# Optimization experiments

Hardware: AMD Instinct MI355X
Metric: run time of the kernel (lower is better)

## Reference

```python
import jax, jax.numpy as jnp
import numpy as np

N = 100000
E = 3200000
IN_C, HID, OUT_C = 256, 32, 16


def gcn_conv(x, W, b, src, dst, n):
    """PyG GCNConv: h = D^{-1/2}(A+I)D^{-1/2} (x W) + b, self-loops already in src/dst."""
    h = x @ W  # [N, out]
    deg = jax.ops.segment_sum(jnp.ones_like(dst, dtype=h.dtype), dst, num_segments=n)
    dinv = jax.lax.rsqrt(deg)  # deg >= 1 because of self-loops
    norm = dinv[src] * dinv[dst]  # [E_all]
    msg = h[src] * norm[:, None]  # gather + normalize
    return jax.ops.segment_sum(msg, dst, num_segments=n) + b


def setup_inputs() -> dict:
    key = jax.random.key(0)
    k1, k2, k3, k4 = jax.random.split(key, 4)
    x = jax.random.normal(k1, (N, IN_C), dtype=jnp.float32)
    edge_index = jax.random.randint(k2, (2, E), 0, N, dtype=jnp.int64)
    # Glorot-ish init for weights, zero bias (as in PyG defaults)
    W1 = jax.random.normal(k3, (IN_C, HID), dtype=jnp.float32) / np.sqrt(IN_C)
    b1 = jnp.zeros((HID,), dtype=jnp.float32)
    W2 = jax.random.normal(k4, (HID, OUT_C), dtype=jnp.float32) / np.sqrt(HID)
    b2 = jnp.zeros((OUT_C,), dtype=jnp.float32)
    return {"x": x, "edge_index": edge_index, "W1": W1, "b1": b1, "W2": W2, "b2": b2}


def reference(x, edge_index, W1, b1, W2, b2):
    n = x.shape[0]
    loops = jnp.arange(n, dtype=edge_index.dtype)
    src = jnp.concatenate([edge_index[0], loops])  # add self-loops
    dst = jnp.concatenate([edge_index[1], loops])
    h = jax.nn.relu(gcn_conv(x, W1, b1, src, dst, n))
    return gcn_conv(h, W2, b2, src, dst, n)
```

## Files before the change

### kernel.cpp

```cpp
#include <hip/hip_runtime.h>

#define IN_C 256
#define HIDC 32
#define OUTC 16
#define NPB  256
#define MAXBKT 800
#define CAP  16384
#define EPB  12288
#define EPT  12

typedef __attribute__((ext_vector_type(8))) short short8;
typedef __attribute__((ext_vector_type(4))) float f32x4;
union S8U4 { short8 s; unsigned u[4]; };

__device__ __forceinline__ unsigned bf16pair(float a, float b) {
    unsigned ua = __float_as_uint(a); ua += 0x7FFF + ((ua >> 16) & 1);
    unsigned ub = __float_as_uint(b); ub += 0x7FFF + ((ub >> 16) & 1);
    return (ua >> 16) | (ub & 0xFFFF0000u);
}
__device__ __forceinline__ float bf16lo(unsigned u) { return __uint_as_float(u << 16); }
__device__ __forceinline__ float bf16hi(unsigned u) { return __uint_as_float(u & 0xFFFF0000u); }
__device__ __forceinline__ unsigned rbf(float a) {
    unsigned u = __float_as_uint(a);
    u += 0x7FFF + ((u >> 16) & 1);
    return u >> 16;
}
__device__ __forceinline__ void split8(const float* xf, short8& hi, short8& lo) {
    S8U4 H, L;
#pragma unroll
    for (int i = 0; i < 4; ++i) {
        float a = xf[2 * i], b = xf[2 * i + 1];
        unsigned ha = rbf(a), hb = rbf(b);
        float ra = a - __uint_as_float(ha << 16);
        float rb = b - __uint_as_float(hb << 16);
        H.u[i] = ha | (hb << 16);
        L.u[i] = rbf(ra) | (rbf(rb) << 16);
    }
    hi = H.s; lo = L.s;
}

__device__ __forceinline__ int edge_at(const int* __restrict__ ei, long long idx, int is64) {
    return is64 ? ei[idx << 1] : ei[idx];
}

__global__ void k_init(const int* __restrict__ ei, int* __restrict__ flag,
                       int* __restrict__ bkt_cur, int nbkt,
                       const float* __restrict__ W1, unsigned short* __restrict__ wf) {
    if (blockIdx.x == 0) {
        __shared__ int nz;
        if (threadIdx.x == 0) nz = 0;
        __syncthreads();
        if (ei[2 * threadIdx.x + 1] != 0) atomicOr(&nz, 1);
        for (int i = threadIdx.x; i < nbkt; i += 256) bkt_cur[i] = i * CAP;
        __syncthreads();
        if (threadIdx.x == 0) *flag = (nz == 0) ? 1 : 0;
    } else {
        int idx = (blockIdx.x - 1) * 256 + threadIdx.x;
        int lane = idx & 63;
        int part = (idx >> 6) & 1;
        int tile = (idx >> 7) & 1;
        int s    = idx >> 8;
        int col = tile * 16 + (lane & 15);
        int k0  = s * 32 + (lane >> 4) * 8;
#pragma unroll
        for (int j = 0; j < 8; ++j) {
            float v = W1[(long long)(k0 + j) * HIDC + col];
            unsigned h = rbf(v);
            float r = v - __uint_as_float(h << 16);
            wf[(long long)idx * 8 + j] = (unsigned short)(part == 0 ? h : rbf(r));
        }
    }
}

__global__ __launch_bounds__(1024) void k_super(const int* __restrict__ ei, long long E,
                                                const int* __restrict__ flag,
                                                int* __restrict__ bkt_cur,
                                                unsigned* __restrict__ packed, int nbkt, int nsb,
                                                const float* __restrict__ x,
                                                const unsigned short* __restrict__ wf,
                                                unsigned short* __restrict__ h1b_us, int n) {
    if ((int)blockIdx.x < nsb) {
        __shared__ int hist[MAXBKT];
        int is64 = *flag;
        for (int i = threadIdx.x; i < nbkt; i += 1024) hist[i] = 0;
        __syncthreads();
        long long lo = (long long)blockIdx.x * EPB;
        int m = (int)((E - lo) < EPB ? (E - lo) : EPB);
        unsigned ew[EPT];
        int      eb[EPT];
#pragma unroll
        for (int j = 0; j < EPT; ++j) {
            int i = j * 1024 + (int)threadIdx.x;
            eb[j] = -1;
            if (i < m) {
                int s = edge_at(ei, lo + i, is64);
                int d = edge_at(ei, E + lo + i, is64);
                ew[j] = (unsigned)s | ((unsigned)(d & (NPB - 1)) << 20);
                eb[j] = d >> 8;
                atomicAdd(&hist[eb[j]], 1);
            }
        }
        __syncthreads();
        for (int b = threadIdx.x; b < nbkt; b += 1024) {
            int c = hist[b];
            hist[b] = c ? atomicAdd(&bkt_cur[b], c) : 0;
        }
        __syncthreads();
#pragma unroll
        for (int j = 0; j < EPT; ++j) {
            if (eb[j] >= 0) {
                int slot = atomicAdd(&hist[eb[j]], 1);
                packed[slot] = ew[j];
            }
        }
    } else {
        const int gb = (int)blockIdx.x - nsb;
        const int t = (int)threadIdx.x;
        const int l = t & 63;
        const int w = t >> 6;
        const long long nb0 = (long long)gb * 256 + w * 16;
        const int kg = l >> 4;
        const long long nodeA = nb0 + (l & 15);
        const bool loadA = nodeA < n;
        f32x4 acc0 = {0.f, 0.f, 0.f, 0.f}, acc1 = {0.f, 0.f, 0.f, 0.f};
#pragma unroll
        for (int s = 0; s < 8; ++s) {
            float xf[8];
            if (loadA) {
                float4 v0 = *(const float4*)(x + nodeA * IN_C + s * 32 + kg * 8);
                float4 v1 = *(const float4*)(x + nodeA * IN_C + s * 32 + kg * 8 + 4);
                xf[0] = v0.x; xf[1] = v0.y; xf[2] = v0.z; xf[3] = v0.w;
                xf[4] = v1.x; xf[5] = v1.y; xf[6] = v1.z; xf[7] = v1.w;
            } else {
#pragma unroll
                for (int j = 0; j < 8; ++j) xf[j] = 0.f;
            }
            short8 ah, al;
            split8(xf, ah, al);
            const unsigned short* base = wf + ((long long)(s * 4) * 64 + l) * 8;
            short8 bh0 = *(const short8*)(base);
            short8 bl0 = *(const short8*)(base + 64 * 8);
            short8 bh1 = *(const short8*)(base + 2 * 64 * 8);
            short8 bl1 = *(const short8*)(base + 3 * 64 * 8);
            acc0 = __builtin_amdgcn_mfma_f32_16x16x32_bf16(ah, bh0, acc0, 0, 0, 0);
            acc0 = __builtin_amdgcn_mfma_f32_16x16x32_bf16(ah, bl0, acc0, 0, 0, 0);
            acc0 = __builtin_amdgcn_mfma_f32_16x16x32_bf16(al, bh0, acc0, 0, 0, 0);
            acc1 = __builtin_amdgcn_mfma_f32_16x16x32_bf16(ah, bh1, acc1, 0, 0, 0);
            acc1 = __builtin_amdgcn_mfma_f32_16x16x32_bf16(ah, bl1, acc1, 0, 0, 0);
            acc1 = __builtin_amdgcn_mfma_f32_16x16x32_bf16(al, bh1, acc1, 0, 0, 0);
        }
#pragma unroll
        for (int r = 0; r < 4; ++r) {
            long long nd = nb0 + (l >> 4) * 4 + r;
            if (nd < n) {
                h1b_us[nd * 32 + (l & 15)]      = (unsigned short)rbf(acc0[r]);
                h1b_us[nd * 32 + 16 + (l & 15)] = (unsigned short)rbf(acc1[r]);
            }
        }
    }
}

__global__ __launch_bounds__(256) void k_bucket_csr(const unsigned* __restrict__ packed,
                                                    const int* __restrict__ bkt_cur,
                                                    int* __restrict__ csr_src,
                                                    int* __restrict__ ptr,
                                                    int* __restrict__ cnt,
                                                    float* __restrict__ dinv,
                                                    unsigned* __restrict__ h1b, int n) {
    __shared__ int hist[NPB];
    __shared__ int off[NPB];
    hist[threadIdx.x] = 0;
    __syncthreads();
    int base = blockIdx.x * CAP;
    int m = bkt_cur[blockIdx.x] - base;
    for (int i = threadIdx.x; i < m; i += 256)
        atomicAdd(&hist[packed[base + i] >> 20], 1);
    __syncthreads();
    off[threadIdx.x] = hist[threadIdx.x];
    __syncthreads();
    for (int o = 1; o < NPB; o <<= 1) {
        int v = (threadIdx.x >= o) ? off[threadIdx.x - o] : 0;
        __syncthreads();
        off[threadIdx.x] += v;
        __syncthreads();
    }
    long long node = (long long)blockIdx.x * NPB + threadIdx.x;
    {
        int exc = off[threadIdx.x] - hist[threadIdx.x];
        if (node < n) {
            float di = rsqrtf((float)hist[threadIdx.x] + 1.0f);
            ptr[node]  = base + exc;
            cnt[node]  = hist[threadIdx.x];
            dinv[node] = di;
            unsigned* row = h1b + node * 16;
#pragma unroll
            for (int q = 0; q < 16; ++q) {
                unsigned u = row[q];
                row[q] = bf16pair(bf16lo(u) * di, bf16hi(u) * di);
            }
        }
        hist[threadIdx.x] = exc;
    }
    __syncthreads();
    for (int i = threadIdx.x; i < m; i += 256) {
        unsigned w = packed[base + i];
        int r = atomicAdd(&hist[w >> 20], 1);
        csr_src[base + r] = (int)(w & 0xFFFFF);
    }
}

__global__ __launch_bounds__(256) void k_agg1g2(const int* __restrict__ ptr,
                                                const int* __restrict__ cnt,
                                                const int* __restrict__ csr_src,
                                                const float* __restrict__ dinv,
                                                const unsigned* __restrict__ h1b,
                                                const float* __restrict__ b1,
                                                const float* __restrict__ W2,
                                                unsigned* __restrict__ h2b, int n) {
    __shared__ float hs[16][33];
    __shared__ float wl2[32][17];
    const int t = threadIdx.x;
    for (int i = t; i < HIDC * OUTC; i += 256) wl2[i >> 4][i & 15] = W2[i];
    const int nl = t >> 4;
    const int cp = t & 15;
    const long long node = (long long)blockIdx.x * 16 + nl;
    float vL = 0.f, vH = 0.f;
    if (node < n) {
        unsigned us = h1b[node * 16 + cp];
        float accL = bf16lo(us), accH = bf16hi(us);
        int st = ptr[node], deg = cnt[node];
        int j = 0;
        for (; j + 3 < deg; j += 4) {
            int s0 = csr_src[st + j], s1 = csr_src[st + j + 1];
            int s2 = csr_src[st + j + 2], s3 = csr_src[st + j + 3];
            unsigned u0 = h1b[(long long)s0 * 16 + cp];
            unsigned u1 = h1b[(long long)s1 * 16 + cp];
            unsigned u2 = h1b[(long long)s2 * 16 + cp];
            unsigned u3 = h1b[(long long)s3 * 16 + cp];
            accL += (bf16lo(u0) + bf16lo(u1)) + (bf16lo(u2) + bf16lo(u3));
            accH += (bf16hi(u0) + bf16hi(u1)) + (bf16hi(u2) + bf16hi(u3));
        }
        for (; j < deg; ++j) {
            unsigned u = h1b[(long long)csr_src[st + j] * 16 + cp];
            accL += bf16lo(u); accH += bf16hi(u);
        }
        float di = dinv[node];
        vL = accL * di + b1[2 * cp];
        vH = accH * di + b1[2 * cp + 1];
        vL = vL > 0.f ? vL : 0.f;
        vH = vH > 0.f ? vH : 0.f;
    }
    hs[nl][2 * cp]     = vL;
    hs[nl][2 * cp + 1] = vH;
    __syncthreads();
    if (t < 128) {
        int nl2 = t >> 3;
        int op  = t & 7;
        long long nd = (long long)blockIdx.x * 16 + nl2;
        if (nd < n) {
            float o0 = 0.f, o1 = 0.f;
#pragma unroll
            for (int k = 0; k < HIDC; ++k) {
                float h = hs[nl2][k];
                o0 = fmaf(h, wl2[k][2 * op],     o0);
                o1 = fmaf(h, wl2[k][2 * op + 1], o1);
            }
            float di = dinv[nd];
            h2b[nd * 8 + op] = bf16pair(o0 * di, o1 * di);
        }
    }
}

__global__ __launch_bounds__(256) void k_agg2csr(const int* __restrict__ ptr,
                                                 const int* __restrict__ cnt,
                                                 const int* __restrict__ csr_src,
                                                 const float* __restrict__ dinv,
                                                 const unsigned* __restrict__ h2b,
                                                 const float* __restrict__ b2,
                                                 float* __restrict__ out, int n) {
    long long g = (long long)blockIdx.x * blockDim.x + threadIdx.x;
    int node = (int)(g >> 3);
    int cp = (int)(g & 7);
    if (node >= n) return;
    unsigned us = h2b[(long long)node * 8 + cp];
    float accL = bf16lo(us), accH = bf16hi(us);
    int st = ptr[node], deg = cnt[node];
    int j = 0;
    for (; j + 3 < deg; j += 4) {
        int s0 = csr_src[st + j], s1 = csr_src[st + j + 1];
        int s2 = csr_src[st + j + 2], s3 = csr_src[st + j + 3];
        unsigned u0 = h2b[(long long)s0 * 8 + cp];
        unsigned u1 = h2b[(long long)s1 * 8 + cp];
        unsigned u2 = h2b[(long long)s2 * 8 + cp];
        unsigned u3 = h2b[(long long)s3 * 8 + cp];
        accL += (bf16lo(u0) + bf16lo(u1)) + (bf16lo(u2) + bf16lo(u3));
        accH += (bf16hi(u0) + bf16hi(u1)) + (bf16hi(u2) + bf16hi(u3));
    }
    for (; j < deg; ++j) {
        unsigned u = h2b[(long long)csr_src[st + j] * 8 + cp];
        accL += bf16lo(u); accH += bf16hi(u);
    }
    float di = dinv[node];
    *(float2*)(out + (long long)node * OUTC + 2 * cp) =
        make_float2(accL * di + b2[2 * cp], accH * di + b2[2 * cp + 1]);
}

extern "C" void kernel_launch(void* const* d_in, const int* in_sizes, int n_in,
                              void* d_out, int out_size, void* d_ws, size_t ws_size,
                              hipStream_t stream) {
    const float* x  = (const float*)d_in[0];
    const int*   ei = (const int*)d_in[1];
    const float* W1 = (const float*)d_in[2];
    const float* b1 = (const float*)d_in[3];
    const float* W2 = (const float*)d_in[4];
    const float* b2 = (const float*)d_in[5];
    const int n = in_sizes[0] / IN_C;
    const long long E = in_sizes[1] / 2;
    float* out = (float*)d_out;

    const int nbkt = (n + NPB - 1) / NPB;
    const int nsb  = (int)((E + EPB - 1) / EPB);
    const int ngb  = (n + 255) / 256;

    char* ws = (char*)d_ws;
    size_t off = 0;
    auto alloc = [&](size_t bytes) { void* p = ws + off; off += (bytes + 255) & ~(size_t)255; return p; };
    int*      flag     = (int*)alloc(256);
    int*      bkt_cur  = (int*)alloc((size_t)MAXBKT * 4);
    float*    dinv     = (float*)alloc((size_t)n * 4);
    int*      cnt      = (int*)alloc((size_t)n * 4);
    int*      ptr      = (int*)alloc((size_t)n * 4);
    unsigned* packed   = (unsigned*)alloc((size_t)nbkt * CAP * 4);
    int*      csr_src  = (int*)alloc((size_t)nbkt * CAP * 4);
    unsigned short* wf = (unsigned short*)alloc(8 * 2 * 2 * 64 * 8 * 2);
    unsigned* h1b      = (unsigned*)alloc((size_t)n * (HIDC / 2) * 4);
    unsigned* h2b      = (unsigned*)alloc((size_t)n * (OUTC / 2) * 4);

    k_init<<<9, 256, 0, stream>>>(ei, flag, bkt_cur, nbkt, W1, wf);
    k_super<<<nsb + ngb, 1024, 0, stream>>>(ei, E, flag, bkt_cur, packed, nbkt, nsb,
                                            x, wf, (unsigned short*)h1b, n);
    k_bucket_csr<<<nbkt, NPB, 0, stream>>>(packed, bkt_cur, csr_src, ptr, cnt, dinv, h1b, n);
    k_agg1g2<<<(n + 15) / 16, 256, 0, stream>>>(ptr, cnt, csr_src, dinv, h1b, b1, W2, h2b, n);
    k_agg2csr<<<(int)(((long long)n * 8 + 255) / 256), 256, 0, stream>>>(
        ptr, cnt, csr_src, dinv, h2b, b2, out, n);
}
```

Before: 161.8 us.

## Replace global bucket atomics with per-block fixed segments and count matrix

The edge-partition pass stops reserving space in each destination bucket with global atomicAdd. Each block now writes its per-bucket counts to a block-by-bucket count matrix and scatters edges into a fixed SEGLEN-slot segment per (bucket, block). The CSR-building kernel prefix-sums its bucket's column of that matrix and uses a binary search to locate each edge. This removes global atomic contention but makes packed reads sparser, adds a search per edge, and silently overflows if any block sends more than SEGLEN edges to one bucket.

```diff
diff --git a/kernel.cpp b/kernel.cpp
--- a/kernel.cpp
+++ b/kernel.cpp
@@ -8,6 +8,7 @@
 #define CAP  16384
 #define EPB  12288
 #define EPT  12
+#define SEGLEN 96
 
 typedef __attribute__((ext_vector_type(8))) short short8;
 typedef __attribute__((ext_vector_type(4))) float f32x4;
@@ -44,14 +45,12 @@
 }
 
 __global__ void k_init(const int* __restrict__ ei, int* __restrict__ flag,
-                       int* __restrict__ bkt_cur, int nbkt,
                        const float* __restrict__ W1, unsigned short* __restrict__ wf) {
     if (blockIdx.x == 0) {
         __shared__ int nz;
         if (threadIdx.x == 0) nz = 0;
         __syncthreads();
         if (ei[2 * threadIdx.x + 1] != 0) atomicOr(&nz, 1);
-        for (int i = threadIdx.x; i < nbkt; i += 256) bkt_cur[i] = i * CAP;
         __syncthreads();
         if (threadIdx.x == 0) *flag = (nz == 0) ? 1 : 0;
     } else {
@@ -74,7 +73,7 @@
 
 __global__ __launch_bounds__(1024) void k_super(const int* __restrict__ ei, long long E,
                                                 const int* __restrict__ flag,
-                                                int* __restrict__ bkt_cur,
+                                                int* __restrict__ cntm,
                                                 unsigned* __restrict__ packed, int nbkt, int nsb,
                                                 const float* __restrict__ x,
                                                 const unsigned short* __restrict__ wf,
@@ -102,15 +101,16 @@
         }
         __syncthreads();
         for (int b = threadIdx.x; b < nbkt; b += 1024) {
-            int c = hist[b];
-            hist[b] = c ? atomicAdd(&bkt_cur[b], c) : 0;
-        }
-        __syncthreads();
+            cntm[(long long)blockIdx.x * nbkt + b] = hist[b];
+            hist[b] = 0;
+        }
+        __syncthreads();
+        const long long segrow = (long long)nsb * SEGLEN;
 #pragma unroll
         for (int j = 0; j < EPT; ++j) {
             if (eb[j] >= 0) {
-                int slot = atomicAdd(&hist[eb[j]], 1);
-                packed[slot] = ew[j];
+                int r = atomicAdd(&hist[eb[j]], 1);
+                packed[(long long)eb[j] * segrow + (long long)blockIdx.x * SEGLEN + r] = ew[j];
             }
         }
     } else {
@@ -161,7 +161,7 @@
 }
 
 __global__ __launch_bounds__(256) void k_bucket_csr(const unsigned* __restrict__ packed,
-                                                    const int* __restrict__ bkt_cur,
+                                                    const int* __restrict__ cntm, int nsb,
                                                     int* __restrict__ csr_src,
                                                     int* __restrict__ ptr,
                                                     int* __restrict__ cnt,
@@ -169,28 +169,54 @@
                                                     unsigned* __restrict__ h1b, int n) {
     __shared__ int hist[NPB];
     __shared__ int off[NPB];
-    hist[threadIdx.x] = 0;
-    __syncthreads();
-    int base = blockIdx.x * CAP;
-    int m = bkt_cur[blockIdx.x] - base;
-    for (int i = threadIdx.x; i < m; i += 256)
-        atomicAdd(&hist[packed[base + i] >> 20], 1);
-    __syncthreads();
-    off[threadIdx.x] = hist[threadIdx.x];
+    __shared__ int P[513];
+    __shared__ int sm[256];
+    const int b = blockIdx.x;
+    const int nbkt = gridDim.x;
+    const int t = threadIdx.x;
+    int e0 = (2 * t < nsb) ? cntm[(long long)(2 * t) * nbkt + b] : 0;
+    int e1 = (2 * t + 1 < nsb) ? cntm[(long long)(2 * t + 1) * nbkt + b] : 0;
+    int pv = e0 + e1;
+    sm[t] = pv;
+    hist[t] = 0;
+    __syncthreads();
+    for (int o = 1; o < 256; o <<= 1) {
+        int v = (t >= o) ? sm[t - o] : 0;
+        __syncthreads();
+        sm[t] += v;
+        __syncthreads();
+    }
+    int pb = sm[t] - pv;
+    if (2 * t < nsb)     P[2 * t]     = pb;
+    if (2 * t + 1 < nsb) P[2 * t + 1] = pb + e0;
+    if (t == 255) P[nsb] = sm[255];
+    __syncthreads();
+    const int m = P[nsb];
+    const long long segrow = (long long)nsb * SEGLEN;
+    const long long pbase = (long long)b * segrow;
+    for (int g = t; g < m; g += 256) {
+        int lo2 = 0, hi2 = nsb;
+        while (hi2 - lo2 > 1) { int mid = (lo2 + hi2) >> 1; if (P[mid] <= g) lo2 = mid; else hi2 = mid; }
+        unsigned w = packed[pbase + (long long)lo2 * SEGLEN + (g - P[lo2])];
+        atomicAdd(&hist[w >> 20], 1);
+    }
+    __syncthreads();
+    off[t] = hist[t];
     __syncthreads();
     for (int o = 1; o < NPB; o <<= 1) {
-        int v = (threadIdx.x >= o) ? off[threadIdx.x - o] : 0;
-        __syncthreads();
-        off[threadIdx.x] += v;
-        __syncthreads();
-    }
-    long long node = (long long)blockIdx.x * NPB + threadIdx.x;
+        int v = (t >= o) ? off[t - o] : 0;
+        __syncthreads();
+        off[t] += v;
+        __syncthreads();
+    }
+    long long node = (long long)b * NPB + t;
+    int base = b * CAP;
     {
-        int exc = off[threadIdx.x] - hist[threadIdx.x];
+        int exc = off[t] - hist[t];
         if (node < n) {
-            float di = rsqrtf((float)hist[threadIdx.x] + 1.0f);
+            float di = rsqrtf((float)hist[t] + 1.0f);
             ptr[node]  = base + exc;
-            cnt[node]  = hist[threadIdx.x];
+            cnt[node]  = hist[t];
             dinv[node] = di;
             unsigned* row = h1b + node * 16;
 #pragma unroll
@@ -199,11 +225,13 @@
                 row[q] = bf16pair(bf16lo(u) * di, bf16hi(u) * di);
             }
         }
-        hist[threadIdx.x] = exc;
-    }
-    __syncthreads();
-    for (int i = threadIdx.x; i < m; i += 256) {
-        unsigned w = packed[base + i];
+        hist[t] = exc;
+    }
+    __syncthreads();
+    for (int g = t; g < m; g += 256) {
+        int lo2 = 0, hi2 = nsb;
+        while (hi2 - lo2 > 1) { int mid = (lo2 + hi2) >> 1; if (P[mid] <= g) lo2 = mid; else hi2 = mid; }
+        unsigned w = packed[pbase + (long long)lo2 * SEGLEN + (g - P[lo2])];
         int r = atomicAdd(&hist[w >> 20], 1);
         csr_src[base + r] = (int)(w & 0xFFFFF);
     }
@@ -326,20 +354,20 @@
     size_t off = 0;
     auto alloc = [&](size_t bytes) { void* p = ws + off; off += (bytes + 255) & ~(size_t)255; return p; };
     int*      flag     = (int*)alloc(256);
-    int*      bkt_cur  = (int*)alloc((size_t)MAXBKT * 4);
     float*    dinv     = (float*)alloc((size_t)n * 4);
     int*      cnt      = (int*)alloc((size_t)n * 4);
     int*      ptr      = (int*)alloc((size_t)n * 4);
-    unsigned* packed   = (unsigned*)alloc((size_t)nbkt * CAP * 4);
+    int*      cntm     = (int*)alloc((size_t)nsb * nbkt * 4);
+    unsigned* packed   = (unsigned*)alloc((size_t)nbkt * nsb * SEGLEN * 4);
     int*      csr_src  = (int*)alloc((size_t)nbkt * CAP * 4);
     unsigned short* wf = (unsigned short*)alloc(8 * 2 * 2 * 64 * 8 * 2);
     unsigned* h1b      = (unsigned*)alloc((size_t)n * (HIDC / 2) * 4);
     unsigned* h2b      = (unsigned*)alloc((size_t)n * (OUTC / 2) * 4);
 
-    k_init<<<9, 256, 0, stream>>>(ei, flag, bkt_cur, nbkt, W1, wf);
-    k_super<<<nsb + ngb, 1024, 0, stream>>>(ei, E, flag, bkt_cur, packed, nbkt, nsb,
+    k_init<<<9, 256, 0, stream>>>(ei, flag, W1, wf);
+    k_super<<<nsb + ngb, 1024, 0, stream>>>(ei, E, flag, cntm, packed, nbkt, nsb,
                                             x, wf, (unsigned short*)h1b, n);
-    k_bucket_csr<<<nbkt, NPB, 0, stream>>>(packed, bkt_cur, csr_src, ptr, cnt, dinv, h1b, n);
+    k_bucket_csr<<<nbkt, NPB, 0, stream>>>(packed, cntm, nsb, csr_src, ptr, cnt, dinv, h1b, n);
     k_agg1g2<<<(n + 15) / 16, 256, 0, stream>>>(ptr, cnt, csr_src, dinv, h1b, b1, W2, h2b, n);
     k_agg2csr<<<(int)(((long long)n * 8 + 255) / 256), 256, 0, stream>>>(
         ptr, cnt, csr_src, dinv, h2b, b2, out, n);
```

Measured after the change: 190.5 us. 1.18x slower.
